# Optimization experiments

Hardware: AMD Instinct MI355X
Metric: run time of the kernel (lower is better)

## Reference

```python
import jax, jax.numpy as jnp
import numpy as np
from jax import lax

MAX_DISP = 4  # correlation window radius -> 9x9 = 81 offsets


def setup_inputs() -> dict:
    key = jax.random.key(0)
    k1, k2 = jax.random.split(key)
    B, C, H, W = 4, 256, 128, 128
    x_1 = jax.random.normal(k1, (B, C, H, W), dtype=jnp.float32)
    x_2 = jax.random.normal(k2, (B, C, H, W), dtype=jnp.float32)
    return {"x_1": x_1, "x_2": x_2}


def reference(x_1, x_2):
    # FlowNet-style correlation: for each displacement (dy, dx) in [-4, 4]^2,
    # out[b, (dy+4)*9 + (dx+4), y, x] = mean_c x1[b,c,y,x] * x2[b,c,y+dy,x+dx]
    # with zero padding of x2 (normalized by C, as in the original CUDA kernel).
    B, C, H, W = x_1.shape
    pad = jnp.pad(x_2, ((0, 0), (0, 0), (MAX_DISP, MAX_DISP), (MAX_DISP, MAX_DISP)))
    outs = []
    for dy in range(2 * MAX_DISP + 1):
        for dx in range(2 * MAX_DISP + 1):
            shifted = lax.dynamic_slice(pad, (0, 0, dy, dx), (B, C, H, W))
            outs.append(jnp.mean(x_1 * shifted, axis=1))  # [B, H, W]
    return jnp.stack(outs, axis=1)  # [B, 81, H, W]
```

## Files before the change

kernel.cpp:

```cpp
#include <hip/hip_runtime.h>


#define MD 4
constexpr int Bc = 4, Cc = 256, Hc = 128, Wc = 128;
constexpr int TH = 16, TW = 16;
constexpr int NDY = 3;
constexpr int CC = 4;
constexpr int SROWS = TH + NDY - 1;
constexpr int SCOLS = TW + 2 * MD;
constexpr int RSC = 48;
constexpr int CH_STRIDE = SROWS * RSC;
constexpr int BUF_DW = CC * CH_STRIDE;
constexpr int NF4 = CC * SROWS * (SCOLS / 4);
constexpr int NTHR = 192;
constexpr int NSLOT = 3;
constexpr int NK = Cc / CC;

__global__ __launch_bounds__(NTHR, 4)
void corr_kernel(const float* __restrict__ x1, const float* __restrict__ x2,
                 float* __restrict__ out)
{
    __shared__ float stg[2 * BUF_DW];

    const int tid  = threadIdx.x;
    const int w    = tid >> 6;
    const int lane = tid & 63;
    const int gy   = lane >> 2;
    const int gx   = lane & 3;

    const int bid  = blockIdx.x;
    const int q    = bid / 24;
    const int r    = bid - q * 24;
    const int g    = r >> 3;
    const int t    = q * 8 + (r & 7);
    const int tx = t & 7;
    const int ty = (t >> 3) & 7;
    const int bb = t >> 6;
    const int x0 = tx * TW, y0 = ty * TH;
    const int rowbase = y0 + 3 * g - MD;

    int  s_goff[NSLOT], s_loff[NSLOT];
    bool s_val[NSLOT], s_act[NSLOT];
    #pragma unroll
    for (int s = 0; s < NSLOT; ++s) {
        int idx = tid + s * NTHR;
        bool active = idx < NF4;
        int i2  = active ? idx : 0;
        int cl  = i2 / (SROWS * 6);
        int rem = i2 - cl * (SROWS * 6);
        int rr  = rem / 6;
        int gc  = rem - rr * 6;
        int yy  = rowbase + rr;
        int xx  = x0 - 4 + 4 * gc;
        s_act[s]  = active;
        s_val[s]  = active && ((unsigned)yy < (unsigned)Hc) && ((unsigned)xx < (unsigned)(Wc - 3));
        s_goff[s] = cl * (Hc * Wc) + yy * Wc + xx;
        s_loff[s] = cl * CH_STRIDE + rr * RSC + 4 * gc;
    }

    const float* x2b = x2 + (size_t)bb * Cc * Hc * Wc;
    const float* x1b = x1 + (((size_t)bb * Cc) * Hc + (y0 + gy)) * Wc + x0 + 4 * gx;

    float acc[9][4];
    #pragma unroll
    for (int dx = 0; dx < 9; ++dx)
        #pragma unroll
        for (int p = 0; p < 4; ++p) acc[dx][p] = 0.f;

    const float4 f40 = make_float4(0.f, 0.f, 0.f, 0.f);
    float4 nf[NSLOT];

    #pragma unroll
    for (int s = 0; s < NSLOT; ++s) {
        nf[s] = f40;
        if (s_val[s]) nf[s] = *(const float4*)(x2b + s_goff[s]);
    }
    #pragma unroll
    for (int s = 0; s < NSLOT; ++s)
        if (s_act[s]) *(float4*)(&stg[s_loff[s]]) = nf[s];

    for (int k = 0; k < NK; ++k) {
        const int pb = k & 1;
        if (k + 1 < NK) {
            const int gof = (k + 1) * CC * Hc * Wc;
            #pragma unroll
            for (int s = 0; s < NSLOT; ++s) {
                nf[s] = f40;
                if (s_val[s]) nf[s] = *(const float4*)(x2b + gof + s_goff[s]);
            }
        }
        __syncthreads();
        #pragma unroll
        for (int cl = 0; cl < CC; ++cl) {
            const int c = k * CC + cl;
            const float4 a4 = *(const float4*)(x1b + c * (Hc * Wc));
            const float* rowp = &stg[pb * BUF_DW + cl * CH_STRIDE + (gy + w) * RSC + 4 * gx];
            const float4 q0 = *(const float4*)(rowp);
            const float4 q1 = *(const float4*)(rowp + 4);
            const float4 q2 = *(const float4*)(rowp + 8);
            const float v[12] = {q0.x, q0.y, q0.z, q0.w,
                                 q1.x, q1.y, q1.z, q1.w,
                                 q2.x, q2.y, q2.z, q2.w};
            const float a[4] = {a4.x, a4.y, a4.z, a4.w};
            #pragma unroll
            for (int dx = 0; dx < 9; ++dx)
                #pragma unroll
                for (int p = 0; p < 4; ++p)
                    acc[dx][p] += a[p] * v[dx + p];
        }
        if (k + 1 < NK) {
            const int lb = ((k + 1) & 1) * BUF_DW;
            #pragma unroll
            for (int s = 0; s < NSLOT; ++s)
                if (s_act[s]) *(float4*)(&stg[lb + s_loff[s]]) = nf[s];
        }
    }

    const float inv = 1.0f / (float)Cc;
    float* ob = out + (((size_t)bb * 81 + (3 * g + w) * 9) * Hc + (y0 + gy)) * Wc + x0 + 4 * gx;
    #pragma unroll
    for (int dx = 0; dx < 9; ++dx) {
        float4 st = make_float4(acc[dx][0] * inv, acc[dx][1] * inv,
                                acc[dx][2] * inv, acc[dx][3] * inv);
        *(float4*)(ob + dx * (Hc * Wc)) = st;
    }
}

extern "C" void kernel_launch(void* const* d_in, const int* in_sizes, int n_in,
                              void* d_out, int out_size, void* d_ws, size_t ws_size,
                              hipStream_t stream) {
    const float* x1 = (const float*)d_in[0];
    const float* x2 = (const float*)d_in[1];
    float* out = (float*)d_out;
    dim3 grid(3 * 8 * 8 * Bc), block(NTHR);
    corr_kernel<<<grid, block, 0, stream>>>(x1, x2, out);
}
```

Measured before the change: 204.0 us.

## Split channel reduction across two thread halves with shared-memory final combine

Doubles the block to 384 threads. Each half reduces over a different half of the 256 channels and stages its own x2 tiles, so the serial channel loop is half as long. The partial sums are combined through shared memory before the output is written. The shared row stride also changes from 48 to 44, likely to reduce bank conflicts, and the occupancy hint rises to 5. This trades more LDS per block and an extra sync-and-reduce step for more parallelism per tile.

```diff
diff --git a/kernel.cpp b/kernel.cpp
--- a/kernel.cpp
+++ b/kernel.cpp
@@ -3,27 +3,31 @@
 
 #define MD 4
 constexpr int Bc = 4, Cc = 256, Hc = 128, Wc = 128;
+constexpr int HW = Hc * Wc;
 constexpr int TH = 16, TW = 16;
 constexpr int NDY = 3;
-constexpr int CC = 4;
+constexpr int NH  = 2;
+constexpr int CC  = 4;
 constexpr int SROWS = TH + NDY - 1;
 constexpr int SCOLS = TW + 2 * MD;
-constexpr int RSC = 48;
+constexpr int RSC = 44;
 constexpr int CH_STRIDE = SROWS * RSC;
-constexpr int BUF_DW = CC * CH_STRIDE;
-constexpr int NF4 = CC * SROWS * (SCOLS / 4);
-constexpr int NTHR = 192;
+constexpr int BUF_DW = NH * CC * CH_STRIDE;
+constexpr int NF4 = NH * CC * SROWS * (SCOLS / 4);
+constexpr int NTHR = 384;
 constexpr int NSLOT = 3;
-constexpr int NK = Cc / CC;
+constexpr int NK = Cc / (NH * CC);
 
-__global__ __launch_bounds__(NTHR, 4)
+__global__ __launch_bounds__(NTHR, 5)
 void corr_kernel(const float* __restrict__ x1, const float* __restrict__ x2,
                  float* __restrict__ out)
 {
     __shared__ float stg[2 * BUF_DW];
 
     const int tid  = threadIdx.x;
-    const int w    = tid >> 6;
+    const int ww   = tid >> 6;
+    const int h    = (ww >= 3) ? 1 : 0;
+    const int w    = ww - 3 * h;
     const int lane = tid & 63;
     const int gy   = lane >> 2;
     const int gx   = lane & 3;
@@ -46,20 +50,22 @@
         int idx = tid + s * NTHR;
         bool active = idx < NF4;
         int i2  = active ? idx : 0;
-        int cl  = i2 / (SROWS * 6);
-        int rem = i2 - cl * (SROWS * 6);
+        int cl8 = i2 / (SROWS * 6);
+        int rem = i2 - cl8 * (SROWS * 6);
         int rr  = rem / 6;
         int gc  = rem - rr * 6;
+        int ch  = (cl8 < CC) ? cl8 : (Cc / 2 + cl8 - CC);
         int yy  = rowbase + rr;
         int xx  = x0 - 4 + 4 * gc;
         s_act[s]  = active;
         s_val[s]  = active && ((unsigned)yy < (unsigned)Hc) && ((unsigned)xx < (unsigned)(Wc - 3));
-        s_goff[s] = cl * (Hc * Wc) + yy * Wc + xx;
-        s_loff[s] = cl * CH_STRIDE + rr * RSC + 4 * gc;
+        s_goff[s] = ch * HW + yy * Wc + xx;
+        s_loff[s] = cl8 * CH_STRIDE + rr * RSC + 4 * gc;
     }
 
-    const float* x2b = x2 + (size_t)bb * Cc * Hc * Wc;
-    const float* x1b = x1 + (((size_t)bb * Cc) * Hc + (y0 + gy)) * Wc + x0 + 4 * gx;
+    const float* x2b = x2 + (size_t)bb * Cc * HW;
+    const float* x1b = x1 + (((size_t)bb * Cc + h * (Cc / 2)) * Hc + (y0 + gy)) * Wc
+                          + x0 + 4 * gx;
 
     float acc[9][4];
     #pragma unroll
@@ -82,7 +88,7 @@
     for (int k = 0; k < NK; ++k) {
         const int pb = k & 1;
         if (k + 1 < NK) {
-            const int gof = (k + 1) * CC * Hc * Wc;
+            const int gof = (k + 1) * CC * HW;
             #pragma unroll
             for (int s = 0; s < NSLOT; ++s) {
                 nf[s] = f40;
@@ -93,8 +99,9 @@
         #pragma unroll
         for (int cl = 0; cl < CC; ++cl) {
             const int c = k * CC + cl;
-            const float4 a4 = *(const float4*)(x1b + c * (Hc * Wc));
-            const float* rowp = &stg[pb * BUF_DW + cl * CH_STRIDE + (gy + w) * RSC + 4 * gx];
+            const float4 a4 = *(const float4*)(x1b + c * HW);
+            const float* rowp = &stg[pb * BUF_DW + (h * CC + cl) * CH_STRIDE
+                                     + (gy + w) * RSC + 4 * gx];
             const float4 q0 = *(const float4*)(rowp);
             const float4 q1 = *(const float4*)(rowp + 4);
             const float4 q2 = *(const float4*)(rowp + 8);
@@ -116,13 +123,28 @@
         }
     }
 
-    const float inv = 1.0f / (float)Cc;
-    float* ob = out + (((size_t)bb * 81 + (3 * g + w) * 9) * Hc + (y0 + gy)) * Wc + x0 + 4 * gx;
-    #pragma unroll
-    for (int dx = 0; dx < 9; ++dx) {
-        float4 st = make_float4(acc[dx][0] * inv, acc[dx][1] * inv,
-                                acc[dx][2] * inv, acc[dx][3] * inv);
-        *(float4*)(ob + dx * (Hc * Wc)) = st;
+    __syncthreads();
+    if (h == 1) {
+        float* dst = &stg[(w * 64 + lane) * 36];
+        #pragma unroll
+        for (int dx = 0; dx < 9; ++dx)
+            #pragma unroll
+            for (int p = 0; p < 4; ++p) dst[dx * 4 + p] = acc[dx][p];
+    }
+    __syncthreads();
+    if (h == 0) {
+        const float inv = 1.0f / (float)Cc;
+        const float* src = &stg[(w * 64 + lane) * 36];
+        float* ob = out + (((size_t)bb * 81 + (3 * g + w) * 9) * Hc + (y0 + gy)) * Wc
+                        + x0 + 4 * gx;
+        #pragma unroll
+        for (int dx = 0; dx < 9; ++dx) {
+            float4 st = make_float4((acc[dx][0] + src[dx * 4 + 0]) * inv,
+                                    (acc[dx][1] + src[dx * 4 + 1]) * inv,
+                                    (acc[dx][2] + src[dx * 4 + 2]) * inv,
+                                    (acc[dx][3] + src[dx * 4 + 3]) * inv);
+            *(float4*)(ob + dx * HW) = st;
+        }
     }
 }
 
```

Measured after the change: 536.4 us. 163% more time.
